# Kernel optimization log

Hardware: AMD Instinct MI355X
Metric: run time of the kernel (lower is better)

## Reference

```python
import jax, jax.numpy as jnp
import numpy as np
from jax import lax

# bior3.5 decomposition low-pass filter (pywt.Wavelet('bior3.5').dec_lo)
_BIOR35_DEC_LO = [-0.013810679320049757, 0.04143203796014927, 0.052480581416189075,
                  -0.26792717880896527, -0.07181553246425873, 0.966747552403483,
                  0.966747552403483, -0.07181553246425873, -0.26792717880896527,
                  0.052480581416189075, 0.04143203796014927, -0.013810679320049757]

J = 3  # decomposition levels


def setup_inputs() -> dict:
    key = jax.random.key(0)
    x = jax.random.normal(key, (16, 64, 16384), dtype=jnp.float32)
    hac = jnp.asarray(np.array(_BIOR35_DEC_LO, dtype=np.float32))
    return {"x": x, "hac": hac}


def _afb1d(x, h0, h1):
    """Analysis filter bank: stride-2 depthwise conv over last dim.

    x: (B, C, N); h0, h1: (L,). Returns (lo, hi), each (B, C, outsize).
    Since every channel uses the same pair of filters, we fold (B, C) into
    the batch dim and run a single-input-channel, 2-output-channel conv.
    """
    B, C, N = x.shape
    L = h0.shape[0]
    outsize = (N + L - 1) // 2              # pywt 'zero' mode coeff length
    p = 2 * (outsize - 1) - N + L           # total padding needed
    if p % 2 == 1:                          # odd -> extra zero on the right
        x = jnp.pad(x, ((0, 0), (0, 0), (0, 1)))
        N += 1
        p -= 1
    half = p // 2
    xr = x.reshape(B * C, 1, N)
    k = jnp.stack([h0, h1])[:, None, :]     # (2, 1, L) -- cross-correlation, like torch
    out = lax.conv_general_dilated(xr, k, window_strides=(2,),
                                   padding=[(half, half)],
                                   dimension_numbers=('NCH', 'OIH', 'NCH'))
    lo = out[:, 0, :].reshape(B, C, outsize)
    hi = out[:, 1, :].reshape(B, C, outsize)
    return lo, hi


def reference(x, hac):
    L = hac.shape[0]
    # QMF pair: h1[i] = (-1)^(i+1) * h0[L-1-i]  (miu[::2] = -1 in torch code)
    sign = jnp.where(jnp.arange(L) % 2 == 0, -1.0, 1.0).astype(hac.dtype)
    h0 = hac
    h1 = hac[::-1] * sign
    x0 = x
    highs = []
    for _ in range(J):
        x0, x1 = _afb1d(x0, h0, h1)
        highs.append(x1)
    return (x0, *highs)
```

## Files before the change

### kernel.cpp

```cpp
#include <hip/hip_runtime.h>


#define FILT_LEN 12
#define ROWS  1024
#define N1    16384
#define O1    8197
#define O2    4104
#define O3    2057
#define NBLK  4
#define T1    2050
#define T2    1026
#define T3    515
#define NTHR  256

#define XCAP   4288
#define L1CAP  2128
#define L2CAP  1072
#define HB1_OFF   0
#define HB2_OFF   2112
#define HB3LO_OFF 3168
#define HB3HI_OFF 3696

__device__ __constant__ const float H0C[FILT_LEN] = {
    -0.013810679320049757f, 0.04143203796014927f, 0.052480581416189075f,
    -0.26792717880896527f, -0.07181553246425873f, 0.966747552403483f,
    0.966747552403483f, -0.07181553246425873f, -0.26792717880896527f,
    0.052480581416189075f, 0.04143203796014927f, -0.013810679320049757f};

__global__ __launch_bounds__(NTHR, 4) void dwt_fused_kernel(
    const float* __restrict__ x,
    float* __restrict__ lo3, float* __restrict__ hi1,
    float* __restrict__ hi2, float* __restrict__ hi3)
{
    __shared__ __align__(16) float xs_lds[XCAP];
    __shared__ __align__(16) float lo1_lds[L1CAP];
    __shared__ __align__(16) float lo2_lds[L2CAP];

    const int b   = blockIdx.x;
    const int row = blockIdx.y;
    const int tid = threadIdx.x;

    float h0[FILT_LEN], h1[FILT_LEN];
#pragma unroll
    for (int i = 0; i < FILT_LEN; ++i) h0[i] = H0C[i];
#pragma unroll
    for (int i = 0; i < FILT_LEN; ++i)
        h1[i] = h0[FILT_LEN - 1 - i] * ((i & 1) ? 1.0f : -1.0f);

    const int s1 = b * T1, e1 = min(s1 + T1, O1);
    const int s2 = b * T2, e2 = min(s2 + T2, O2);
    const int s3 = b * T3, e3 = min(s3 + T3, O3);
    const int c2s = max(0, min(s2, 2 * s3 - 10));
    const int c2e = min(O2, max(e2, 2 * e3));
    const int c1s = max(0, min(s1, 2 * c2s - 10)) & ~1;
    const int c1e = min(O1, max(e1, 2 * c2e));
    const int span1 = c1e - c1s;
    const int span2 = c2e - c2s;
    const int span3 = e3 - s3;
    const int xbase = 2 * c1s - 12;

    const int d2raw = 2 * c2s - 10 - c1s + 12;
    const int PAD1  = 12 + (d2raw & 2);
    const int DELTA2 = d2raw + (d2raw & 2);
    const int d3raw = 2 * s3 - 10 - c2s + 12;
    const int PAD2  = 12 + (d3raw & 2);
    const int DELTA3 = d3raw + (d3raw & 2);

    const float* xrow = x + (size_t)row * N1;

    {
        const float4 z4 = make_float4(0.f, 0.f, 0.f, 0.f);
        float4* l1p = reinterpret_cast<float4*>(lo1_lds);
        float4* l2p = reinterpret_cast<float4*>(lo2_lds);
#pragma unroll 2
        for (int i = tid; i < (L1CAP + L2CAP) / 4; i += NTHR) {
            if (i < L1CAP / 4) l1p[i] = z4;
            else               l2p[i - L1CAP / 4] = z4;
        }
        float4* xp = reinterpret_cast<float4*>(xs_lds);
        for (int i = tid; i < XCAP / 4; i += NTHR) {
            const int g0 = xbase + 4 * i;
            float4 v;
            if (g0 >= 0 && g0 + 4 <= N1) {
                v = *reinterpret_cast<const float4*>(&xrow[g0]);
            } else {
                v.x = (g0 + 0 >= 0 && g0 + 0 < N1) ? xrow[g0 + 0] : 0.f;
                v.y = (g0 + 1 >= 0 && g0 + 1 < N1) ? xrow[g0 + 1] : 0.f;
                v.z = (g0 + 2 >= 0 && g0 + 2 < N1) ? xrow[g0 + 2] : 0.f;
                v.w = (g0 + 3 >= 0 && g0 + 3 < N1) ? xrow[g0 + 3] : 0.f;
            }
            xp[i] = v;
        }
    }
    __syncthreads();

    float hr1[2][8];
#pragma unroll
    for (int r = 0; r < 2; ++r) {
        const int tt0 = tid * 8 + r * 2048;
        if (tt0 < span1) {
            float w[28];
            const float4* wp = reinterpret_cast<const float4*>(&xs_lds[2 * tt0]);
#pragma unroll
            for (int m = 0; m < 7; ++m) {
                const float4 v = wp[m];
                w[4 * m + 0] = v.x; w[4 * m + 1] = v.y;
                w[4 * m + 2] = v.z; w[4 * m + 3] = v.w;
            }
            float a0[8], a1[8];
#pragma unroll
            for (int k = 0; k < 8; ++k) { a0[k] = 0.f; a1[k] = 0.f; }
#pragma unroll
            for (int l = 0; l < FILT_LEN; ++l) {
#pragma unroll
                for (int k = 0; k < 8; ++k) {
                    const float v = w[2 * k + 2 + l];
                    a0[k] = fmaf(v, h0[l], a0[k]);
                    a1[k] = fmaf(v, h1[l], a1[k]);
                }
            }
            if (tt0 + 8 <= span1) {
#pragma unroll
                for (int k = 0; k < 8; ++k) lo1_lds[tt0 + k + PAD1] = a0[k];
            } else {
#pragma unroll
                for (int k = 0; k < 8; ++k)
                    if (tt0 + k < span1) lo1_lds[tt0 + k + PAD1] = a0[k];
            }
#pragma unroll
            for (int k = 0; k < 8; ++k) hr1[r][k] = a1[k];
        }
    }
    __syncthreads();

#pragma unroll
    for (int r = 0; r < 2; ++r) {
        const int tt0 = tid * 8 + r * 2048;
        if (tt0 < span1) {
            if (tt0 + 8 <= span1) {
                float4* hp = reinterpret_cast<float4*>(&xs_lds[HB1_OFF + tt0]);
                hp[0] = make_float4(hr1[r][0], hr1[r][1], hr1[r][2], hr1[r][3]);
                hp[1] = make_float4(hr1[r][4], hr1[r][5], hr1[r][6], hr1[r][7]);
            } else {
#pragma unroll
                for (int k = 0; k < 8; ++k)
                    if (tt0 + k < span1) xs_lds[HB1_OFF + tt0 + k] = hr1[r][k];
            }
        }
    }
    float hr2[2][4];
#pragma unroll
    for (int r = 0; r < 2; ++r) {
        const int tt0 = tid * 4 + r * 1024;
        if (tt0 < span2) {
            float w[20];
            const float4* wp = reinterpret_cast<const float4*>(&lo1_lds[2 * tt0 + DELTA2]);
#pragma unroll
            for (int m = 0; m < 5; ++m) {
                const float4 v = wp[m];
                w[4 * m + 0] = v.x; w[4 * m + 1] = v.y;
                w[4 * m + 2] = v.z; w[4 * m + 3] = v.w;
            }
            float a0[4], a1[4];
#pragma unroll
            for (int k = 0; k < 4; ++k) { a0[k] = 0.f; a1[k] = 0.f; }
#pragma unroll
            for (int l = 0; l < FILT_LEN; ++l) {
#pragma unroll
                for (int k = 0; k < 4; ++k) {
                    const float v = w[2 * k + l];
                    a0[k] = fmaf(v, h0[l], a0[k]);
                    a1[k] = fmaf(v, h1[l], a1[k]);
                }
            }
#pragma unroll
            for (int k = 0; k < 4; ++k)
                if (tt0 + k < span2) lo2_lds[tt0 + k + PAD2] = a0[k];
#pragma unroll
            for (int k = 0; k < 4; ++k) hr2[r][k] = a1[k];
        }
    }
    __syncthreads();

    {
        float* dst = hi1 + (size_t)row * O1;
        const int i0 = s1 - c1s, ie = e1 - c1s;
        for (int i = i0 + tid; i < ie; i += NTHR)
            dst[c1s + i] = xs_lds[HB1_OFF + i];
    }
#pragma unroll
    for (int r = 0; r < 2; ++r) {
        const int tt0 = tid * 4 + r * 1024;
        if (tt0 < span2) {
            if (tt0 + 4 <= span2) {
                *reinterpret_cast<float4*>(&xs_lds[HB2_OFF + tt0]) =
                    make_float4(hr2[r][0], hr2[r][1], hr2[r][2], hr2[r][3]);
            } else {
#pragma unroll
                for (int k = 0; k < 4; ++k)
                    if (tt0 + k < span2) xs_lds[HB2_OFF + tt0 + k] = hr2[r][k];
            }
        }
    }
#pragma unroll
    for (int r = 0; r < 2; ++r) {
        const int tt0 = tid * 2 + r * 512;
        if (tt0 < span3) {
            float w[16];
            const float4* wp = reinterpret_cast<const float4*>(&lo2_lds[2 * tt0 + DELTA3]);
#pragma unroll
            for (int m = 0; m < 4; ++m) {
                const float4 v = wp[m];
                w[4 * m + 0] = v.x; w[4 * m + 1] = v.y;
                w[4 * m + 2] = v.z; w[4 * m + 3] = v.w;
            }
            float a0[2], a1[2];
#pragma unroll
            for (int k = 0; k < 2; ++k) { a0[k] = 0.f; a1[k] = 0.f; }
#pragma unroll
            for (int l = 0; l < FILT_LEN; ++l) {
#pragma unroll
                for (int k = 0; k < 2; ++k) {
                    const float v = w[2 * k + l];
                    a0[k] = fmaf(v, h0[l], a0[k]);
                    a1[k] = fmaf(v, h1[l], a1[k]);
                }
            }
#pragma unroll
            for (int k = 0; k < 2; ++k) {
                if (tt0 + k < span3) {
                    xs_lds[HB3LO_OFF + tt0 + k] = a0[k];
                    xs_lds[HB3HI_OFF + tt0 + k] = a1[k];
                }
            }
        }
    }
    __syncthreads();

    {
        float* dst = hi2 + (size_t)row * O2;
        const int i0 = s2 - c2s, ie = e2 - c2s;
        for (int i = i0 + tid; i < ie; i += NTHR)
            dst[c2s + i] = xs_lds[HB2_OFF + i];
    }
    {
        float* dlo = lo3 + (size_t)row * O3 + s3;
        float* dhi = hi3 + (size_t)row * O3 + s3;
        for (int i = tid; i < span3; i += NTHR) {
            dlo[i] = xs_lds[HB3LO_OFF + i];
            dhi[i] = xs_lds[HB3HI_OFF + i];
        }
    }
}

extern "C" void kernel_launch(void* const* d_in, const int* in_sizes, int n_in,
                              void* d_out, int out_size, void* d_ws, size_t ws_size,
                              hipStream_t stream)
{
    const float* x = (const float*)d_in[0];
    float* out = (float*)d_out;

    float* lo3 = out;
    float* hi1 = out + (size_t)ROWS * O3;
    float* hi2 = hi1 + (size_t)ROWS * O1;
    float* hi3 = hi2 + (size_t)ROWS * O2;

    dwt_fused_kernel<<<dim3(NBLK, ROWS), dim3(NTHR), 0, stream>>>(
        x, lo3, hi1, hi2, hi3);
}
```

Before: 135.2 us.

## Swizzle LDS layout, specialize per-block constants, shrink shared memory footprint

Adds an XOR swizzle on float4 indices for all shared-memory buffers to reduce bank conflicts on the strided float4 reads and writes. Block-dependent offsets become compile-time constants through a template per blockIdx.x, which also drops the boundary checks on interior loads. Level-2 and level-3 intermediates are packed into the existing buffers, so the separate lo2 array goes away, only the pad regions are zeroed instead of the whole buffers, and launch bounds rise to 6 blocks per CU. The cost is four code copies and more complex, alignment-sensitive indexing.

```diff
diff --git a/kernel.cpp b/kernel.cpp
--- a/kernel.cpp
+++ b/kernel.cpp
@@ -14,96 +14,107 @@
 #define NTHR  256
 
 #define XCAP   4288
-#define L1CAP  2128
-#define L2CAP  1072
-#define HB1_OFF   0
-#define HB2_OFF   2112
-#define HB3LO_OFF 3168
-#define HB3HI_OFF 3696
-
-__device__ __constant__ const float H0C[FILT_LEN] = {
-    -0.013810679320049757f, 0.04143203796014927f, 0.052480581416189075f,
-    -0.26792717880896527f, -0.07181553246425873f, 0.966747552403483f,
-    0.966747552403483f, -0.07181553246425873f, -0.26792717880896527f,
-    0.052480581416189075f, 0.04143203796014927f, -0.013810679320049757f};
-
-__global__ __launch_bounds__(NTHR, 4) void dwt_fused_kernel(
-    const float* __restrict__ x,
-    float* __restrict__ lo3, float* __restrict__ hi1,
-    float* __restrict__ hi2, float* __restrict__ hi3)
+#define L1CAP  2112
+#define LO2_OFF  2112
+#define HB2_OFF  3200
+#define LO3_OFF  0
+#define HI3_OFF  544
+
+constexpr int cmin(int a, int b) { return a < b ? a : b; }
+constexpr int cmax(int a, int b) { return a > b ? a : b; }
+
+__device__ __forceinline__ int sw4(int f4) { return f4 ^ ((f4 >> 3) & 7); }
+__device__ __forceinline__ float4 ld4(const float* p, int f4) {
+    return reinterpret_cast<const float4*>(p)[sw4(f4)];
+}
+__device__ __forceinline__ void st4(float* p, int f4, float4 v) {
+    reinterpret_cast<float4*>(p)[sw4(f4)] = v;
+}
+__device__ __forceinline__ float ldss(const float* p, int j) {
+    return p[(sw4(j >> 2) << 2) | (j & 3)];
+}
+__device__ __forceinline__ void stss(float* p, int j, float v) {
+    p[(sw4(j >> 2) << 2) | (j & 3)] = v;
+}
+
+__device__ __forceinline__ float h0tap(int i) {
+    constexpr float H[FILT_LEN] = {
+        -0.013810679320049757f, 0.04143203796014927f, 0.052480581416189075f,
+        -0.26792717880896527f, -0.07181553246425873f, 0.966747552403483f,
+        0.966747552403483f, -0.07181553246425873f, -0.26792717880896527f,
+        0.052480581416189075f, 0.04143203796014927f, -0.013810679320049757f};
+    return H[i];
+}
+
+template<int B>
+struct Cfg {
+    static constexpr int s1 = B * T1, e1 = cmin(s1 + T1, O1);
+    static constexpr int s2 = B * T2, e2 = cmin(s2 + T2, O2);
+    static constexpr int s3 = B * T3, e3 = cmin(s3 + T3, O3);
+    static constexpr int c2s = cmax(0, cmin(s2, 2 * s3 - 10));
+    static constexpr int c2e = cmin(O2, cmax(e2, 2 * e3));
+    static constexpr int c1s = cmax(0, cmin(s1, 2 * c2s - 10)) & ~1;
+    static constexpr int c1e = cmin(O1, cmax(e1, 2 * c2e));
+    static constexpr int span1 = c1e - c1s;
+    static constexpr int span2 = c2e - c2s;
+    static constexpr int span3 = e3 - s3;
+    static constexpr int xbase = 2 * c1s - 12;
+    static constexpr int D2 = 2 * c2s - 10 - c1s + 12;
+    static constexpr int ab2 = D2 & ~3, p2 = D2 & 3;
+    static constexpr int D3 = 2 * s3 - 10 - c2s + 12;
+    static constexpr int ab3 = D3 & ~3, p3 = D3 & 3;
+    static constexpr int zt1 = 2104 - (12 + span1);
+    static constexpr int zt2 = 1056 - (12 + span2);
+};
+
+template<int B>
+__device__ __forceinline__ void body(
+    const float* __restrict__ xrow,
+    float* __restrict__ lo3r, float* __restrict__ hi1r,
+    float* __restrict__ hi2r, float* __restrict__ hi3r,
+    float* __restrict__ xs, float* __restrict__ l1, const int tid)
 {
-    __shared__ __align__(16) float xs_lds[XCAP];
-    __shared__ __align__(16) float lo1_lds[L1CAP];
-    __shared__ __align__(16) float lo2_lds[L2CAP];
-
-    const int b   = blockIdx.x;
-    const int row = blockIdx.y;
-    const int tid = threadIdx.x;
+    using C = Cfg<B>;
 
     float h0[FILT_LEN], h1[FILT_LEN];
 #pragma unroll
-    for (int i = 0; i < FILT_LEN; ++i) h0[i] = H0C[i];
-#pragma unroll
-    for (int i = 0; i < FILT_LEN; ++i)
-        h1[i] = h0[FILT_LEN - 1 - i] * ((i & 1) ? 1.0f : -1.0f);
-
-    const int s1 = b * T1, e1 = min(s1 + T1, O1);
-    const int s2 = b * T2, e2 = min(s2 + T2, O2);
-    const int s3 = b * T3, e3 = min(s3 + T3, O3);
-    const int c2s = max(0, min(s2, 2 * s3 - 10));
-    const int c2e = min(O2, max(e2, 2 * e3));
-    const int c1s = max(0, min(s1, 2 * c2s - 10)) & ~1;
-    const int c1e = min(O1, max(e1, 2 * c2e));
-    const int span1 = c1e - c1s;
-    const int span2 = c2e - c2s;
-    const int span3 = e3 - s3;
-    const int xbase = 2 * c1s - 12;
-
-    const int d2raw = 2 * c2s - 10 - c1s + 12;
-    const int PAD1  = 12 + (d2raw & 2);
-    const int DELTA2 = d2raw + (d2raw & 2);
-    const int d3raw = 2 * s3 - 10 - c2s + 12;
-    const int PAD2  = 12 + (d3raw & 2);
-    const int DELTA3 = d3raw + (d3raw & 2);
-
-    const float* xrow = x + (size_t)row * N1;
-
-    {
-        const float4 z4 = make_float4(0.f, 0.f, 0.f, 0.f);
-        float4* l1p = reinterpret_cast<float4*>(lo1_lds);
-        float4* l2p = reinterpret_cast<float4*>(lo2_lds);
-#pragma unroll 2
-        for (int i = tid; i < (L1CAP + L2CAP) / 4; i += NTHR) {
-            if (i < L1CAP / 4) l1p[i] = z4;
-            else               l2p[i - L1CAP / 4] = z4;
-        }
-        float4* xp = reinterpret_cast<float4*>(xs_lds);
+    for (int i = 0; i < FILT_LEN; ++i) {
+        h0[i] = h0tap(i);
+        h1[i] = h0tap(FILT_LEN - 1 - i) * ((i & 1) ? 1.0f : -1.0f);
+    }
+
+    if constexpr (C::xbase >= 0 && C::xbase + XCAP <= N1) {
+        for (int i = tid; i < XCAP / 4; i += NTHR)
+            st4(xs, i, *reinterpret_cast<const float4*>(xrow + C::xbase + 4 * i));
+    } else {
         for (int i = tid; i < XCAP / 4; i += NTHR) {
-            const int g0 = xbase + 4 * i;
+            const int g0 = C::xbase + 4 * i;
             float4 v;
             if (g0 >= 0 && g0 + 4 <= N1) {
-                v = *reinterpret_cast<const float4*>(&xrow[g0]);
-            } else {
-                v.x = (g0 + 0 >= 0 && g0 + 0 < N1) ? xrow[g0 + 0] : 0.f;
-                v.y = (g0 + 1 >= 0 && g0 + 1 < N1) ? xrow[g0 + 1] : 0.f;
-                v.z = (g0 + 2 >= 0 && g0 + 2 < N1) ? xrow[g0 + 2] : 0.f;
-                v.w = (g0 + 3 >= 0 && g0 + 3 < N1) ? xrow[g0 + 3] : 0.f;
-            }
-            xp[i] = v;
-        }
-    }
+                v = *reinterpret_cast<const float4*>(xrow + g0);
+            } else {
+                v.x = ((unsigned)(g0 + 0) < (unsigned)N1) ? xrow[g0 + 0] : 0.f;
+                v.y = ((unsigned)(g0 + 1) < (unsigned)N1) ? xrow[g0 + 1] : 0.f;
+                v.z = ((unsigned)(g0 + 2) < (unsigned)N1) ? xrow[g0 + 2] : 0.f;
+                v.w = ((unsigned)(g0 + 3) < (unsigned)N1) ? xrow[g0 + 3] : 0.f;
+            }
+            st4(xs, i, v);
+        }
+    }
+    if (tid < 12)      stss(l1, tid, 0.f);
+    if (tid < C::zt1)  stss(l1, 12 + C::span1 + tid, 0.f);
     __syncthreads();
 
     float hr1[2][8];
 #pragma unroll
     for (int r = 0; r < 2; ++r) {
         const int tt0 = tid * 8 + r * 2048;
-        if (tt0 < span1) {
+        if (tt0 < C::span1) {
             float w[28];
-            const float4* wp = reinterpret_cast<const float4*>(&xs_lds[2 * tt0]);
+            const int f0 = tid * 4 + r * 1024;
 #pragma unroll
             for (int m = 0; m < 7; ++m) {
-                const float4 v = wp[m];
+                const float4 v = ld4(xs, f0 + m);
                 w[4 * m + 0] = v.x; w[4 * m + 1] = v.y;
                 w[4 * m + 2] = v.z; w[4 * m + 3] = v.w;
             }
@@ -119,13 +130,15 @@
                     a1[k] = fmaf(v, h1[l], a1[k]);
                 }
             }
-            if (tt0 + 8 <= span1) {
-#pragma unroll
-                for (int k = 0; k < 8; ++k) lo1_lds[tt0 + k + PAD1] = a0[k];
+            if (tt0 + 8 <= C::span1) {
+                st4(l1, 3 + tid * 2 + r * 512,
+                    make_float4(a0[0], a0[1], a0[2], a0[3]));
+                st4(l1, 4 + tid * 2 + r * 512,
+                    make_float4(a0[4], a0[5], a0[6], a0[7]));
             } else {
 #pragma unroll
                 for (int k = 0; k < 8; ++k)
-                    if (tt0 + k < span1) lo1_lds[tt0 + k + PAD1] = a0[k];
+                    if (tt0 + k < C::span1) stss(l1, 12 + tt0 + k, a0[k]);
             }
 #pragma unroll
             for (int k = 0; k < 8; ++k) hr1[r][k] = a1[k];
@@ -136,28 +149,32 @@
 #pragma unroll
     for (int r = 0; r < 2; ++r) {
         const int tt0 = tid * 8 + r * 2048;
-        if (tt0 < span1) {
-            if (tt0 + 8 <= span1) {
-                float4* hp = reinterpret_cast<float4*>(&xs_lds[HB1_OFF + tt0]);
-                hp[0] = make_float4(hr1[r][0], hr1[r][1], hr1[r][2], hr1[r][3]);
-                hp[1] = make_float4(hr1[r][4], hr1[r][5], hr1[r][6], hr1[r][7]);
+        if (tt0 < C::span1) {
+            if (tt0 + 8 <= C::span1) {
+                st4(xs, tid * 2 + r * 512,
+                    make_float4(hr1[r][0], hr1[r][1], hr1[r][2], hr1[r][3]));
+                st4(xs, tid * 2 + r * 512 + 1,
+                    make_float4(hr1[r][4], hr1[r][5], hr1[r][6], hr1[r][7]));
             } else {
 #pragma unroll
                 for (int k = 0; k < 8; ++k)
-                    if (tt0 + k < span1) xs_lds[HB1_OFF + tt0 + k] = hr1[r][k];
-            }
-        }
-    }
+                    if (tt0 + k < C::span1) stss(xs, tt0 + k, hr1[r][k]);
+            }
+        }
+    }
+    if (tid < 12)      stss(xs, LO2_OFF + tid, 0.f);
+    if (tid < C::zt2)  stss(xs, LO2_OFF + 12 + C::span2 + tid, 0.f);
+
     float hr2[2][4];
 #pragma unroll
     for (int r = 0; r < 2; ++r) {
         const int tt0 = tid * 4 + r * 1024;
-        if (tt0 < span2) {
+        if (tt0 < C::span2) {
             float w[20];
-            const float4* wp = reinterpret_cast<const float4*>(&lo1_lds[2 * tt0 + DELTA2]);
+            const int f0 = tid * 2 + r * 512 + (C::ab2 >> 2);
 #pragma unroll
             for (int m = 0; m < 5; ++m) {
-                const float4 v = wp[m];
+                const float4 v = ld4(l1, f0 + m);
                 w[4 * m + 0] = v.x; w[4 * m + 1] = v.y;
                 w[4 * m + 2] = v.z; w[4 * m + 3] = v.w;
             }
@@ -168,49 +185,52 @@
             for (int l = 0; l < FILT_LEN; ++l) {
 #pragma unroll
                 for (int k = 0; k < 4; ++k) {
-                    const float v = w[2 * k + l];
+                    const float v = w[2 * k + l + C::p2];
                     a0[k] = fmaf(v, h0[l], a0[k]);
                     a1[k] = fmaf(v, h1[l], a1[k]);
                 }
             }
-#pragma unroll
-            for (int k = 0; k < 4; ++k)
-                if (tt0 + k < span2) lo2_lds[tt0 + k + PAD2] = a0[k];
+            if (tt0 + 4 <= C::span2) {
+                st4(xs, 531 + tid + r * 256,
+                    make_float4(a0[0], a0[1], a0[2], a0[3]));
+            } else {
+#pragma unroll
+                for (int k = 0; k < 4; ++k)
+                    if (tt0 + k < C::span2) stss(xs, LO2_OFF + 12 + tt0 + k, a0[k]);
+            }
 #pragma unroll
             for (int k = 0; k < 4; ++k) hr2[r][k] = a1[k];
         }
     }
     __syncthreads();
 
-    {
-        float* dst = hi1 + (size_t)row * O1;
-        const int i0 = s1 - c1s, ie = e1 - c1s;
-        for (int i = i0 + tid; i < ie; i += NTHR)
-            dst[c1s + i] = xs_lds[HB1_OFF + i];
-    }
+    for (int i = (C::s1 - C::c1s) + tid; i < C::e1 - C::c1s; i += NTHR)
+        hi1r[C::c1s + i] = ldss(xs, i);
+
 #pragma unroll
     for (int r = 0; r < 2; ++r) {
         const int tt0 = tid * 4 + r * 1024;
-        if (tt0 < span2) {
-            if (tt0 + 4 <= span2) {
-                *reinterpret_cast<float4*>(&xs_lds[HB2_OFF + tt0]) =
-                    make_float4(hr2[r][0], hr2[r][1], hr2[r][2], hr2[r][3]);
+        if (tt0 < C::span2) {
+            if (tt0 + 4 <= C::span2) {
+                st4(xs, (HB2_OFF >> 2) + tid + r * 256,
+                    make_float4(hr2[r][0], hr2[r][1], hr2[r][2], hr2[r][3]));
             } else {
 #pragma unroll
                 for (int k = 0; k < 4; ++k)
-                    if (tt0 + k < span2) xs_lds[HB2_OFF + tt0 + k] = hr2[r][k];
-            }
-        }
-    }
+                    if (tt0 + k < C::span2) stss(xs, HB2_OFF + tt0 + k, hr2[r][k]);
+            }
+        }
+    }
+
 #pragma unroll
     for (int r = 0; r < 2; ++r) {
         const int tt0 = tid * 2 + r * 512;
-        if (tt0 < span3) {
+        if (tt0 < C::span3) {
             float w[16];
-            const float4* wp = reinterpret_cast<const float4*>(&lo2_lds[2 * tt0 + DELTA3]);
+            const int f0 = (LO2_OFF >> 2) + tid + r * 256 + (C::ab3 >> 2);
 #pragma unroll
             for (int m = 0; m < 4; ++m) {
-                const float4 v = wp[m];
+                const float4 v = ld4(xs, f0 + m);
                 w[4 * m + 0] = v.x; w[4 * m + 1] = v.y;
                 w[4 * m + 2] = v.z; w[4 * m + 3] = v.w;
             }
@@ -221,35 +241,51 @@
             for (int l = 0; l < FILT_LEN; ++l) {
 #pragma unroll
                 for (int k = 0; k < 2; ++k) {
-                    const float v = w[2 * k + l];
+                    const float v = w[2 * k + l + C::p3];
                     a0[k] = fmaf(v, h0[l], a0[k]);
                     a1[k] = fmaf(v, h1[l], a1[k]);
                 }
             }
 #pragma unroll
             for (int k = 0; k < 2; ++k) {
-                if (tt0 + k < span3) {
-                    xs_lds[HB3LO_OFF + tt0 + k] = a0[k];
-                    xs_lds[HB3HI_OFF + tt0 + k] = a1[k];
+                if (tt0 + k < C::span3) {
+                    stss(l1, LO3_OFF + tt0 + k, a0[k]);
+                    stss(l1, HI3_OFF + tt0 + k, a1[k]);
                 }
             }
         }
     }
     __syncthreads();
 
-    {
-        float* dst = hi2 + (size_t)row * O2;
-        const int i0 = s2 - c2s, ie = e2 - c2s;
-        for (int i = i0 + tid; i < ie; i += NTHR)
-            dst[c2s + i] = xs_lds[HB2_OFF + i];
-    }
-    {
-        float* dlo = lo3 + (size_t)row * O3 + s3;
-        float* dhi = hi3 + (size_t)row * O3 + s3;
-        for (int i = tid; i < span3; i += NTHR) {
-            dlo[i] = xs_lds[HB3LO_OFF + i];
-            dhi[i] = xs_lds[HB3HI_OFF + i];
-        }
+    for (int i = (C::s2 - C::c2s) + tid; i < C::e2 - C::c2s; i += NTHR)
+        hi2r[C::c2s + i] = ldss(xs, HB2_OFF + i);
+    for (int i = tid; i < C::span3; i += NTHR) {
+        lo3r[C::s3 + i] = ldss(l1, LO3_OFF + i);
+        hi3r[C::s3 + i] = ldss(l1, HI3_OFF + i);
+    }
+}
+
+__global__ __launch_bounds__(NTHR, 6) void dwt_fused_kernel(
+    const float* __restrict__ x,
+    float* __restrict__ lo3, float* __restrict__ hi1,
+    float* __restrict__ hi2, float* __restrict__ hi3)
+{
+    __shared__ __align__(16) float xs[XCAP];
+    __shared__ __align__(16) float l1[L1CAP];
+
+    const int row = blockIdx.y;
+    const int tid = threadIdx.x;
+    const float* xrow = x + (size_t)row * N1;
+    float* lo3r = lo3 + (size_t)row * O3;
+    float* hi1r = hi1 + (size_t)row * O1;
+    float* hi2r = hi2 + (size_t)row * O2;
+    float* hi3r = hi3 + (size_t)row * O3;
+
+    switch (blockIdx.x) {
+        case 0:  body<0>(xrow, lo3r, hi1r, hi2r, hi3r, xs, l1, tid); break;
+        case 1:  body<1>(xrow, lo3r, hi1r, hi2r, hi3r, xs, l1, tid); break;
+        case 2:  body<2>(xrow, lo3r, hi1r, hi2r, hi3r, xs, l1, tid); break;
+        default: body<3>(xrow, lo3r, hi1r, hi2r, hi3r, xs, l1, tid); break;
     }
 }
 
```

Result: faster. 120.2 us (-11.1%).
